# Kernel optimization log

Hardware: AMD Instinct MI355X
Metric: run time of the kernel (lower is better)

The kernel has to match this reference:

```python
import jax, jax.numpy as jnp
import numpy as np


def conv2d(x, w, pad=1):
    return jax.lax.conv_general_dilated(
        x, w, (1, 1), [(pad, pad), (pad, pad)],
        dimension_numbers=('NCHW', 'OIHW', 'NCHW'))


def bn(x, g, b, m, v, eps=1e-5):
    inv = g / jnp.sqrt(v + eps)
    return x * inv[None, :, None, None] + (b - m * inv)[None, :, None, None]


def deform_conv(x, wp, bp, wd):
    # v2-style DeformConv2D: internal p_conv -> offsets, bilinear sample, 3x3 conv
    b, c, h, w = x.shape
    ks = 3
    N = ks * ks
    offset = conv2d(x, wp, 1) + bp[None, :, None, None]   # (b, 2N, h, w)
    xp = jnp.pad(x, ((0, 0), (0, 0), (1, 1), (1, 1)))     # zero_padding(1)
    Hp, Wp = h + 2, w + 2
    off = offset.transpose(0, 2, 3, 1)                    # (b, h, w, 2N)
    pn_y, pn_x = jnp.meshgrid(jnp.arange(-1, 2), jnp.arange(-1, 2), indexing='ij')
    # sampling locations p = p_0 + p_n + offset (in padded coords)
    py = jnp.arange(1, h + 1)[None, :, None, None] + pn_y.reshape(-1)[None, None, None, :] + off[..., :N]
    px = jnp.arange(1, w + 1)[None, None, :, None] + pn_x.reshape(-1)[None, None, None, :] + off[..., N:]
    fy = jnp.floor(jax.lax.stop_gradient(py))
    fx = jnp.floor(jax.lax.stop_gradient(px))
    qy0 = jnp.clip(fy, 0, Hp - 1); qy1 = jnp.clip(fy + 1, 0, Hp - 1)
    qx0 = jnp.clip(fx, 0, Wp - 1); qx1 = jnp.clip(fx + 1, 0, Wp - 1)
    py = jnp.clip(py, 0, Hp - 1); px = jnp.clip(px, 0, Wp - 1)
    g_lt = (1 + (qy0 - py)) * (1 + (qx0 - px))
    g_rb = (1 - (qy1 - py)) * (1 - (qx1 - px))
    g_lb = (1 + (qy0 - py)) * (1 - (qx1 - px))
    g_rt = (1 - (qy1 - py)) * (1 + (qx0 - px))
    flat = xp.reshape(b, c, Hp * Wp)

    def gather(qy, qx):
        idx = (qy * Wp + qx).astype(jnp.int32).reshape(b, 1, -1)
        return jnp.take_along_axis(flat, idx, axis=2).reshape(b, c, h, w, N)

    x_off = (g_lt[:, None] * gather(qy0, qx0) + g_rb[:, None] * gather(qy1, qx1)
             + g_lb[:, None] * gather(qy0, qx1) + g_rt[:, None] * gather(qy1, qx0))
    outc = wd.shape[0]
    # equivalent to _reshape_x_offset + Conv2d(kernel=ks, stride=ks)
    return jnp.einsum('bchwn,ocn->bohw', x_off, wd.reshape(outc, c, N))


def setup_inputs() -> dict:
    key = jax.random.key(0)
    ks = jax.random.split(key, 24)
    B, H, W = 256, 28, 28

    def nrm(k, s, sc=1.0):
        return jax.random.normal(k, s, jnp.float32) * sc

    return {
        'x': nrm(ks[0], (B, 3, H, W)),
        'w1': nrm(ks[1], (32, 3, 3, 3), 0.2),
        'g1': jax.random.uniform(ks[2], (32,), jnp.float32) + 0.5,
        'b1': nrm(ks[3], (32,), 0.1),
        'm1': nrm(ks[4], (32,), 0.1),
        'v1': jax.random.uniform(ks[5], (32,), jnp.float32) + 0.5,
        'wp': nrm(ks[6], (18, 32, 3, 3), 0.01),  # p_conv: small offsets
        'bp': nrm(ks[7], (18,), 0.1),
        'w2': nrm(ks[8], (32, 32, 3, 3), 0.1),
        'g2': jax.random.uniform(ks[9], (32,), jnp.float32) + 0.5,
        'b2': nrm(ks[10], (32,), 0.1),
        'm2': nrm(ks[11], (32,), 0.1),
        'v2': jax.random.uniform(ks[12], (32,), jnp.float32) + 0.5,
        'w3': nrm(ks[13], (64, 32, 3, 3), 0.1),
        'g3': jax.random.uniform(ks[14], (64,), jnp.float32) + 0.5,
        'b3': nrm(ks[15], (64,), 0.1),
        'm3': nrm(ks[16], (64,), 0.1),
        'v3': jax.random.uniform(ks[17], (64,), jnp.float32) + 0.5,
        'wc': nrm(ks[18], (10, 64), 0.1),
        'bc': nrm(ks[19], (10,), 0.1),
    }


def reference(x, w1, g1, b1, m1, v1, wp, bp, w2, g2, b2, m2, v2,
              w3, g3, b3, m3, v3, wc, bc):
    h = bn(jax.nn.relu(conv2d(x, w1)), g1, b1, m1, v1)
    h = bn(jax.nn.relu(deform_conv(h, wp, bp, w2)), g2, b2, m2, v2)
    h = bn(jax.nn.relu(conv2d(h, w3)), g3, b3, m3, v3)
    h = h.mean(axis=(2, 3))               # avg_pool2d(28) on 28x28 -> global mean
    logits = h @ wc.T + bc
    return jax.nn.log_softmax(logits, axis=1)
```

## Files before the change

### kernel.cpp

```cpp
#include <hip/hip_runtime.h>
#include <hip/hip_bf16.h>
#include <math.h>

typedef __attribute__((ext_vector_type(8))) short short8;
typedef __attribute__((ext_vector_type(8))) _Float16 half8;
typedef __attribute__((ext_vector_type(4))) float floatx4;

#define NB 256
#define NW 12
#define NT (NW * 64)

#define WPB_OFF 0u
#define W2B_OFF 18432u
#define W3B_OFF 36864u
#define W1B_OFF 73728u
#define C1S_OFF 75776u
#define C2S_OFF 75904u
#define C3S_OFF 76032u

#define L_IMG1 0
#define L_U    50240
#define L_OFFT 100480
#define L_WL   125056
#define L_TOT  162944


#define LDS_FENCE() __asm__ volatile("" ::: "memory")

static __device__ __forceinline__ unsigned short f2h(float f) {
    _Float16 h = (_Float16)f;
    unsigned short u;
    __builtin_memcpy(&u, &h, 2);
    return u;
}
static __device__ __forceinline__ float h2f(unsigned short u) {
    _Float16 h;
    __builtin_memcpy(&h, &u, 2);
    return (float)h;
}

static __device__ __forceinline__ unsigned pkh(float a, float b) {
    _Float16 ha = (_Float16)a, hb = (_Float16)b;
    unsigned short ua, ub;
    __builtin_memcpy(&ua, &ha, 2);
    __builtin_memcpy(&ub, &hb, 2);
    return (unsigned)ua | ((unsigned)ub << 16);
}

static __device__ __forceinline__ half8 h8(uint4 u) {
    half8 r;
    __builtin_memcpy(&r, &u, 16);
    return r;
}

static __device__ __forceinline__ unsigned pkmul_l(unsigned a, unsigned b) {
    unsigned d;
    asm("v_pk_mul_f16 %0, %1, %2 op_sel:[0,0] op_sel_hi:[0,1]"
        : "=v"(d) : "v"(a), "v"(b));
    return d;
}
static __device__ __forceinline__ unsigned pkfma_l(unsigned a, unsigned b, unsigned c) {
    unsigned d;
    asm("v_pk_fma_f16 %0, %1, %2, %3 op_sel:[0,0,0] op_sel_hi:[0,1,1]"
        : "=v"(d) : "v"(a), "v"(b), "v"(c));
    return d;
}
static __device__ __forceinline__ unsigned pkfma_h(unsigned a, unsigned b, unsigned c) {
    unsigned d;
    asm("v_pk_fma_f16 %0, %1, %2, %3 op_sel:[1,0,0] op_sel_hi:[1,1,1]"
        : "=v"(d) : "v"(a), "v"(b), "v"(c));
    return d;
}

__global__ void wcvt(const float* __restrict__ wp, const float* __restrict__ w2,
                     const float* __restrict__ w3, const float* __restrict__ w1,
                     const float* __restrict__ g1, const float* __restrict__ b1,
                     const float* __restrict__ m1, const float* __restrict__ v1,
                     const float* __restrict__ g2, const float* __restrict__ b2,
                     const float* __restrict__ m2, const float* __restrict__ v2,
                     const float* __restrict__ g3, const float* __restrict__ b3,
                     const float* __restrict__ m3, const float* __restrict__ v3,
                     unsigned short* __restrict__ wpb, unsigned short* __restrict__ w2b,
                     unsigned short* __restrict__ w3b, unsigned short* __restrict__ w1b,
                     float* __restrict__ c1s, float* __restrict__ c2s,
                     float* __restrict__ c3s)
{
    int t = blockIdx.x * 256 + threadIdx.x;
    if (t < 9216) {
        int oc = t / 288, k = t % 288;
        int n = k >> 5, ic = k & 31;
        wpb[t] = (oc < 18) ? f2h(wp[oc * 288 + ic * 9 + n]) : (unsigned short)0;
    } else if (t < 18432) {
        int i = t - 9216;
        int oc = i / 288, k = i % 288;
        int n = k >> 5, ic = k & 31;
        float inv = g2[oc] * rsqrtf(v2[oc] + 1e-5f);
        w2b[i] = f2h(w2[oc * 288 + ic * 9 + n] * inv);
    } else if (t < 36864) {
        int i = t - 18432;
        int oc = i / 288, k = i % 288;
        int n = k >> 5, ic = k & 31;
        float inv = g3[oc] * rsqrtf(v3[oc] + 1e-5f);
        w3b[i] = f2h(w3[oc * 288 + ic * 9 + n] * inv);
    } else if (t < 37888) {
        int i = t - 36864;
        int oc = i >> 5, k = i & 31;
        int n = k / 3, ic = k - n * 3;
        float inv = g1[oc] * rsqrtf(v1[oc] + 1e-5f);
        w1b[i] = (k < 27) ? f2h(w1[oc * 27 + ic * 9 + n] * inv) : (unsigned short)0;
    } else if (t < 37920) {
        int c = t - 37888;
        float inv = g1[c] * rsqrtf(v1[c] + 1e-5f);
        c1s[c] = b1[c] - m1[c] * inv;
    } else if (t < 37952) {
        int c = t - 37920;
        float inv = g2[c] * rsqrtf(v2[c] + 1e-5f);
        c2s[c] = b2[c] - m2[c] * inv;
    } else if (t < 38016) {
        int c = t - 37952;
        float inv = g3[c] * rsqrtf(v3[c] + 1e-5f);
        c3s[c] = b3[c] - m3[c] * inv;
    }
}

__global__ __launch_bounds__(NT, 3) void meganet(
    const float* __restrict__ x,
    const unsigned short* __restrict__ wpb, const unsigned short* __restrict__ w2b,
    const unsigned short* __restrict__ w3b, const unsigned short* __restrict__ w1b,
    const float* __restrict__ c1s, const float* __restrict__ c2s,
    const float* __restrict__ c3s, const float* __restrict__ bp,
    const float* __restrict__ wc, const float* __restrict__ bc,
    float* __restrict__ outp)
{
    __shared__ __align__(16) unsigned char ALL[L_TOT];
    int t = threadIdx.x, b = blockIdx.x;
    int w = t >> 6, l = t & 63, col = l & 15, q = l >> 4;
    int qs = q << 4;
    int chxA = ((col >> 3) << 4) | ((col & 7) * 2);
    int chxB = ((((16 + col) >> 3) & 3) << 4) | ((col & 7) * 2);

    unsigned char* img1 = ALL + L_IMG1;
    unsigned char* uimg = ALL + L_U;

    {
        const float4* xg = (const float4*)(x + (size_t)b * 2352);
        float4* xl = (float4*)uimg;
        for (int i = t; i < 588; i += NT) xl[i] = xg[i];
    }
    {
        const uint4* s1 = (const uint4*)wpb;
        const uint4* s2 = (const uint4*)w2b;
        for (int i = t; i < 2304; i += NT) {
            int row = i / 36, g = i - row * 36;
            uint4 v = (row < 32) ? s1[row * 36 + g] : s2[(row - 32) * 36 + g];
            *(uint4*)(ALL + L_WL + row * 592 + g * 16) = v;
        }
        if (t < 128) *(uint4*)(ALL + L_OFFT + t * 16) = ((const uint4*)w1b)[t];
    }
    if (t == 700) ((float*)uimg)[2352] = 0.f;
    if (t < 4)  *(uint4*)(img1 + 784 * 64 + t * 16) = make_uint4(0u, 0u, 0u, 0u);
    if (t >= 4 && t < 8) *(uint4*)(uimg + 784 * 64 + (t - 4) * 16) = make_uint4(0u, 0u, 0u, 0u);

    float s0 = c1s[col], s1v = c1s[16 + col];
    float bias0 = bp[col];
    float bias1 = (col < 2) ? bp[16 + col] : 0.f;
    float sh0 = c2s[col], sh1 = c2s[16 + col];

    __syncthreads();

    {
        half8 bf0 = h8(*(const uint4*)(ALL + L_OFFT + col * 64 + q * 16));
        half8 bf1 = h8(*(const uint4*)(ALL + L_OFFT + (16 + col) * 64 + q * 16));
        const float* xs = (const float*)uimg;
        for (int mt = w; mt < 49; mt += NW) {
            int p = mt * 16 + col;
            int y = p / 28, xx = p % 28;
            unsigned au[4];
#pragma unroll
            for (int jp = 0; jp < 4; jp++) {
                float vv[2];
#pragma unroll
                for (int h = 0; h < 2; h++) {
                    int k = q * 8 + jp * 2 + h;
                    int n = k / 3, ic = k - n * 3;
                    int yy = y + n / 3 - 1, xc = xx + n % 3 - 1;
                    bool ok = (k < 27) && ((unsigned)yy < 28u) && ((unsigned)xc < 28u);
                    int idx = ok ? (ic * 784 + yy * 28 + xc) : 2352;
                    vv[h] = xs[idx];
                }
                au[jp] = pkh(vv[0], vv[1]);
            }
            uint4 a4 = make_uint4(au[0], au[1], au[2], au[3]);
            half8 a = h8(a4);
            floatx4 d0 = {0.f, 0.f, 0.f, 0.f}, d1 = {0.f, 0.f, 0.f, 0.f};
            d0 = __builtin_amdgcn_mfma_f32_16x16x32_f16(a, bf0, d0, 0, 0, 0);
            d1 = __builtin_amdgcn_mfma_f32_16x16x32_f16(a, bf1, d1, 0, 0, 0);
#pragma unroll
            for (int r = 0; r < 4; r++) {
                int pout = mt * 16 + q * 4 + r;
                int sp = (pout << 6) | ((pout & 6) << 3);
                *(unsigned short*)(img1 + (sp ^ chxA)) = f2h(fmaxf(d0[r], 0.f) + s0);
                *(unsigned short*)(img1 + (sp ^ chxB)) = f2h(fmaxf(d1[r], 0.f) + s1v);
            }
        }
    }
    __syncthreads();

    {
        const unsigned char* ib = img1;
        unsigned char* wsc = ALL + L_OFFT + w * 1536;
        unsigned short* otw = (unsigned short*)wsc;
        unsigned char* gscr = wsc + 576;

        half8 b2fr[18];
#pragma unroll
        for (int n = 0; n < 9; n++) {
            b2fr[n]     = h8(*(const uint4*)(ALL + L_WL + (32 + col) * 592 + n * 64 + q * 16));
            b2fr[9 + n] = h8(*(const uint4*)(ALL + L_WL + (48 + col) * 592 + n * 64 + q * 16));
        }

        for (int mt = w; mt < 49; mt += NW) {
            int p = mt * 16 + col;
            int y = p / 28, xx = p % 28;

            floatx4 a0 = {0.f, 0.f, 0.f, 0.f}, a1 = {0.f, 0.f, 0.f, 0.f};
#pragma unroll
            for (int n = 0; n < 9; n++) {
                int yy = y + n / 3 - 1, xc = xx + n % 3 - 1;
                bool ok = ((unsigned)yy < 28u) && ((unsigned)xc < 28u);
                int tp = ok ? (yy * 28 + xc) : 784;
                int sp = (tp << 6) | ((tp & 6) << 3);
                half8 a  = h8(*(const uint4*)(ib + (sp ^ qs)));
                half8 p0 = h8(*(const uint4*)(ALL + L_WL + col * 592 + n * 64 + q * 16));
                half8 p1 = h8(*(const uint4*)(ALL + L_WL + (16 + col) * 592 + n * 64 + q * 16));
                a0 = __builtin_amdgcn_mfma_f32_16x16x32_f16(a, p0, a0, 0, 0, 0);
                a1 = __builtin_amdgcn_mfma_f32_16x16x32_f16(a, p1, a1, 0, 0, 0);
            }
#pragma unroll
            for (int r = 0; r < 4; r++)
                otw[(q * 4 + r) * 18 + col] = f2h(a0[r] + bias0);
            if (col < 2) {
#pragma unroll
                for (int r = 0; r < 4; r++)
                    otw[(q * 4 + r) * 18 + 16 + col] = f2h(a1[r] + bias1);
            }
            LDS_FENCE();

            floatx4 d0 = {0.f, 0.f, 0.f, 0.f}, d1 = {0.f, 0.f, 0.f, 0.f};
#pragma unroll
            for (int tg = 0; tg < 3; tg++) {
                if (l < 48) {
                    int px = l & 15, n = tg * 3 + (l >> 4);
                    int pg = mt * 16 + px;
                    int yg = pg / 28, xg = pg % 28;
                    float offy = h2f(otw[px * 18 + n]);
                    float offx = h2f(otw[px * 18 + 9 + n]);
                    float py = (float)(yg + n / 3) + offy;
                    float pxf = (float)(xg + n % 3) + offx;
                    float fy = floorf(py), fx = floorf(pxf);
                    float qy0 = fminf(fmaxf(fy, 0.f), 29.f);
                    float qy1 = fminf(fmaxf(fy + 1.f, 0.f), 29.f);
                    float qx0 = fminf(fmaxf(fx, 0.f), 29.f);
                    float qx1 = fminf(fmaxf(fx + 1.f, 0.f), 29.f);
                    float pyc = fminf(fmaxf(py, 0.f), 29.f);
                    float pxc = fminf(fmaxf(pxf, 0.f), 29.f);
                    float glt = (1.f + (qy0 - pyc)) * (1.f + (qx0 - pxc));
                    float grb = (1.f - (qy1 - pyc)) * (1.f - (qx1 - pxc));
                    float glb = (1.f + (qy0 - pyc)) * (1.f - (qx1 - pxc));
                    float grt = (1.f - (qy1 - pyc)) * (1.f + (qx0 - pxc));
                    int iy0 = (int)qy0, iy1 = (int)qy1, ix0 = (int)qx0, ix1 = (int)qx1;
                    int ly0 = iy0 - 1, ly1 = iy1 - 1, lx0 = ix0 - 1, lx1 = ix1 - 1;
                    bool v00 = ((unsigned)ly0 < 28u) && ((unsigned)lx0 < 28u);
                    bool v11 = ((unsigned)ly1 < 28u) && ((unsigned)lx1 < 28u);
                    bool v01 = ((unsigned)ly0 < 28u) && ((unsigned)lx1 < 28u);
                    bool v10 = ((unsigned)ly1 < 28u) && ((unsigned)lx0 < 28u);
                    unsigned p00 = v00 ? (unsigned)(ly0 * 28 + lx0) : 784u;
                    unsigned p11 = v11 ? (unsigned)(ly1 * 28 + lx1) : 784u;
                    unsigned p01 = v01 ? (unsigned)(ly0 * 28 + lx1) : 784u;
                    unsigned p10 = v10 ? (unsigned)(ly1 * 28 + lx0) : 784u;
                    unsigned s00 = (p00 << 6) | ((p00 & 6u) << 3);
                    unsigned s11 = (p11 << 6) | ((p11 & 6u) << 3);
                    unsigned s01 = (p01 << 6) | ((p01 & 6u) << 3);
                    unsigned s10 = (p10 << 6) | ((p10 & 6u) << 3);
                    uint4 rec = make_uint4(pkh(glt, grb), pkh(glb, grt),
                                           s00 | (s11 << 16), s01 | (s10 << 16));
                    *(uint4*)(gscr + l * 16) = rec;
                }
                LDS_FENCE();

#pragma unroll
                for (int k3 = 0; k3 < 3; k3++) {
                    int n = tg * 3 + k3;
                    uint4 rec = *(const uint4*)(gscr + (k3 * 16 + col) * 16);
                    unsigned o00 = (rec.z & 0xffffu) ^ qs, o11 = (rec.z >> 16) ^ qs;
                    unsigned o01 = (rec.w & 0xffffu) ^ qs, o10 = (rec.w >> 16) ^ qs;
                    uint4 u00 = *(const uint4*)(ib + o00);
                    uint4 u11 = *(const uint4*)(ib + o11);
                    uint4 u01 = *(const uint4*)(ib + o01);
                    uint4 u10 = *(const uint4*)(ib + o10);
                    unsigned f0 = pkfma_h(rec.y, u10.x,
                                  pkfma_l(rec.y, u01.x,
                                  pkfma_h(rec.x, u11.x,
                                  pkmul_l(rec.x, u00.x))));
                    unsigned f1 = pkfma_h(rec.y, u10.y,
                                  pkfma_l(rec.y, u01.y,
                                  pkfma_h(rec.x, u11.y,
                                  pkmul_l(rec.x, u00.y))));
                    unsigned f2 = pkfma_h(rec.y, u10.z,
                                  pkfma_l(rec.y, u01.z,
                                  pkfma_h(rec.x, u11.z,
                                  pkmul_l(rec.x, u00.z))));
                    unsigned f3 = pkfma_h(rec.y, u10.w,
                                  pkfma_l(rec.y, u01.w,
                                  pkfma_h(rec.x, u11.w,
                                  pkmul_l(rec.x, u00.w))));
                    uint4 af4 = make_uint4(f0, f1, f2, f3);
                    half8 af = h8(af4);
                    d0 = __builtin_amdgcn_mfma_f32_16x16x32_f16(af, b2fr[n], d0, 0, 0, 0);
                    d1 = __builtin_amdgcn_mfma_f32_16x16x32_f16(af, b2fr[9 + n], d1, 0, 0, 0);
                }
            }
#pragma unroll
            for (int r = 0; r < 4; r++) {
                int pout = mt * 16 + q * 4 + r;
                int sp = (pout << 6) | ((pout & 6) << 3);
                *(unsigned short*)(uimg + (sp ^ chxA)) = f2h(fmaxf(d0[r], 0.f) + sh0);
                *(unsigned short*)(uimg + (sp ^ chxB)) = f2h(fmaxf(d1[r], 0.f) + sh1);
            }
        }
    }
    __syncthreads();

    {
        const uint4* src = (const uint4*)w3b;
        for (int i = t; i < 2304; i += NT) {
            int row = i / 36, g = i - row * 36;
            *(uint4*)(ALL + L_WL + row * 592 + g * 16) = src[row * 36 + g];
        }
    }
    __syncthreads();

    {
        float* part = (float*)(ALL + L_OFFT);
        int ocp = w & 1;
        const unsigned char* ib = uimg;

        half8 wfr[18];
#pragma unroll
        for (int n = 0; n < 9; n++) {
            wfr[n]     = h8(*(const uint4*)(ALL + L_WL + (ocp * 32 + col) * 592 + n * 64 + q * 16));
            wfr[9 + n] = h8(*(const uint4*)(ALL + L_WL + (ocp * 32 + 16 + col) * 592 + n * 64 + q * 16));
        }

        float psA = 0.f, psB = 0.f;
        for (int mt = (w >> 1); mt < 49; mt += (NW / 2)) {
            int p = mt * 16 + col;
            int y = p / 28, xx = p % 28;
            floatx4 cA = {0.f, 0.f, 0.f, 0.f}, cB = {0.f, 0.f, 0.f, 0.f};
#pragma unroll
            for (int n = 0; n < 9; n++) {
                int yy = y + n / 3 - 1, xc = xx + n % 3 - 1;
                bool ok = ((unsigned)yy < 28u) && ((unsigned)xc < 28u);
                int tp = ok ? (yy * 28 + xc) : 784;
                int sp = (tp << 6) | ((tp & 6) << 3);
                half8 a = h8(*(const uint4*)(ib + (sp ^ qs)));
                cA = __builtin_amdgcn_mfma_f32_16x16x32_f16(a, wfr[n], cA, 0, 0, 0);
                cB = __builtin_amdgcn_mfma_f32_16x16x32_f16(a, wfr[9 + n], cB, 0, 0, 0);
            }
            psA += fmaxf(cA[0], 0.f) + fmaxf(cA[1], 0.f) + fmaxf(cA[2], 0.f) + fmaxf(cA[3], 0.f);
            psB += fmaxf(cB[0], 0.f) + fmaxf(cB[1], 0.f) + fmaxf(cB[2], 0.f) + fmaxf(cB[3], 0.f);
        }
        psA += __shfl_xor(psA, 16, 64); psA += __shfl_xor(psA, 32, 64);
        psB += __shfl_xor(psB, 16, 64); psB += __shfl_xor(psB, 32, 64);
        if (l < 16) { part[w * 32 + l] = psA; part[w * 32 + 16 + l] = psB; }
    }
    __syncthreads();

    if (t < 64) {
        const float* part = (const float*)(ALL + L_OFFT);
        int hi = t >> 5, c = t & 31;
        float s = 0.f;
#pragma unroll
        for (int j = 0; j < NW / 2; j++) s += part[(2 * j + hi) * 32 + c];
        float feat = s * (1.f / 784.f) + c3s[t];
        float lg[10];
        float mx = -1e30f;
#pragma unroll
        for (int j = 0; j < 10; j++) {
            float v = feat * wc[j * 64 + t];
            v += __shfl_xor(v, 1, 64);  v += __shfl_xor(v, 2, 64);
            v += __shfl_xor(v, 4, 64);  v += __shfl_xor(v, 8, 64);
            v += __shfl_xor(v, 16, 64); v += __shfl_xor(v, 32, 64);
            lg[j] = v + bc[j];
            mx = fmaxf(mx, lg[j]);
        }
        float se = 0.f;
#pragma unroll
        for (int j = 0; j < 10; j++) se += expf(lg[j] - mx);
        float lse = logf(se);
#pragma unroll
        for (int j = 0; j < 10; j++)
            if (t == j) outp[(size_t)b * 10 + j] = lg[j] - mx - lse;
    }
}

extern "C" void kernel_launch(void* const* d_in, const int* in_sizes, int n_in,
                              void* d_out, int out_size, void* d_ws, size_t ws_size,
                              hipStream_t stream)
{
    (void)in_sizes; (void)n_in; (void)out_size; (void)ws_size;
    const float* x  = (const float*)d_in[0];
    const float* w1 = (const float*)d_in[1];
    const float* g1 = (const float*)d_in[2];
    const float* b1 = (const float*)d_in[3];
    const float* m1 = (const float*)d_in[4];
    const float* v1 = (const float*)d_in[5];
    const float* wp = (const float*)d_in[6];
    const float* bp = (const float*)d_in[7];
    const float* w2 = (const float*)d_in[8];
    const float* g2 = (const float*)d_in[9];
    const float* b2 = (const float*)d_in[10];
    const float* m2 = (const float*)d_in[11];
    const float* v2 = (const float*)d_in[12];
    const float* w3 = (const float*)d_in[13];
    const float* g3 = (const float*)d_in[14];
    const float* b3 = (const float*)d_in[15];
    const float* m3 = (const float*)d_in[16];
    const float* v3 = (const float*)d_in[17];
    const float* wc = (const float*)d_in[18];
    const float* bc = (const float*)d_in[19];
    float* outp = (float*)d_out;

    unsigned char* ws = (unsigned char*)d_ws;
    unsigned short* wpb = (unsigned short*)(ws + WPB_OFF);
    unsigned short* w2b = (unsigned short*)(ws + W2B_OFF);
    unsigned short* w3b = (unsigned short*)(ws + W3B_OFF);
    unsigned short* w1b = (unsigned short*)(ws + W1B_OFF);
    float* c1s = (float*)(ws + C1S_OFF);
    float* c2s = (float*)(ws + C2S_OFF);
    float* c3s = (float*)(ws + C3S_OFF);

    wcvt<<<149, 256, 0, stream>>>(wp, w2, w3, w1, g1, b1, m1, v1,
                                  g2, b2, m2, v2, g3, b3, m3, v3,
                                  wpb, w2b, w3b, w1b, c1s, c2s, c3s);
    meganet<<<NB, NT, 0, stream>>>(x, wpb, w2b, w3b, w1b, c1s, c2s, c3s,
                                   bp, wc, bc, outp);
}
```

Before: 128.1 us.

## Share conv3 A-fragment across all 64 outputs and transpose offset scratch layout

The conv3 stage now has each wave compute all four 16-channel output groups for a tile, reading weights from LDS per tap instead of splitting output channels across wave pairs. This reuses the activation fragment four times and halves redundant A loads. In the offset conv, p0 weights are hoisted into registers, p1 loads are limited to the two useful lanes, and offsets are stored channel-major with vector stores. The cost is more LDS weight traffic per MFMA in conv3 and a different work split across waves (49 tiles over 12 waves).

New measurement: 134.5 us. 1.05x slower.

```diff
diff --git a/kernel.cpp b/kernel.cpp
--- a/kernel.cpp
+++ b/kernel.cpp
@@ -5,6 +5,7 @@
 typedef __attribute__((ext_vector_type(8))) short short8;
 typedef __attribute__((ext_vector_type(8))) _Float16 half8;
 typedef __attribute__((ext_vector_type(4))) float floatx4;
+typedef __attribute__((ext_vector_type(4))) unsigned short ushort4v;
 
 #define NB 256
 #define NW 12
@@ -23,6 +24,7 @@
 #define L_OFFT 100480
 #define L_WL   125056
 #define L_TOT  162944
+
 
 
 #define LDS_FENCE() __asm__ volatile("" ::: "memory")
@@ -213,8 +215,10 @@
         unsigned char* gscr = wsc + 576;
 
         half8 b2fr[18];
+        half8 p0fr[9];
 #pragma unroll
         for (int n = 0; n < 9; n++) {
+            p0fr[n]     = h8(*(const uint4*)(ALL + L_WL + col * 592 + n * 64 + q * 16));
             b2fr[n]     = h8(*(const uint4*)(ALL + L_WL + (32 + col) * 592 + n * 64 + q * 16));
             b2fr[9 + n] = h8(*(const uint4*)(ALL + L_WL + (48 + col) * 592 + n * 64 + q * 16));
         }
@@ -230,19 +234,24 @@
                 bool ok = ((unsigned)yy < 28u) && ((unsigned)xc < 28u);
                 int tp = ok ? (yy * 28 + xc) : 784;
                 int sp = (tp << 6) | ((tp & 6) << 3);
-                half8 a  = h8(*(const uint4*)(ib + (sp ^ qs)));
-                half8 p0 = h8(*(const uint4*)(ALL + L_WL + col * 592 + n * 64 + q * 16));
-                half8 p1 = h8(*(const uint4*)(ALL + L_WL + (16 + col) * 592 + n * 64 + q * 16));
-                a0 = __builtin_amdgcn_mfma_f32_16x16x32_f16(a, p0, a0, 0, 0, 0);
-                a1 = __builtin_amdgcn_mfma_f32_16x16x32_f16(a, p1, a1, 0, 0, 0);
-            }
-#pragma unroll
-            for (int r = 0; r < 4; r++)
-                otw[(q * 4 + r) * 18 + col] = f2h(a0[r] + bias0);
-            if (col < 2) {
-#pragma unroll
-                for (int r = 0; r < 4; r++)
-                    otw[(q * 4 + r) * 18 + 16 + col] = f2h(a1[r] + bias1);
+                half8 a = h8(*(const uint4*)(ib + (sp ^ qs)));
+                a0 = __builtin_amdgcn_mfma_f32_16x16x32_f16(a, p0fr[n], a0, 0, 0, 0);
+                half8 p1v = h8(make_uint4(0u, 0u, 0u, 0u));
+                if (col < 2)
+                    p1v = h8(*(const uint4*)(ALL + L_WL + (16 + col) * 592 + n * 64 + q * 16));
+                a1 = __builtin_amdgcn_mfma_f32_16x16x32_f16(a, p1v, a1, 0, 0, 0);
+            }
+            {
+                ushort4v ov;
+                ov[0] = f2h(a0[0] + bias0); ov[1] = f2h(a0[1] + bias0);
+                ov[2] = f2h(a0[2] + bias0); ov[3] = f2h(a0[3] + bias0);
+                *(ushort4v*)(otw + col * 16 + q * 4) = ov;
+                if (col < 2) {
+                    ushort4v ov1;
+                    ov1[0] = f2h(a1[0] + bias1); ov1[1] = f2h(a1[1] + bias1);
+                    ov1[2] = f2h(a1[2] + bias1); ov1[3] = f2h(a1[3] + bias1);
+                    *(ushort4v*)(otw + (16 + col) * 16 + q * 4) = ov1;
+                }
             }
             LDS_FENCE();
 
@@ -253,8 +262,8 @@
                     int px = l & 15, n = tg * 3 + (l >> 4);
                     int pg = mt * 16 + px;
                     int yg = pg / 28, xg = pg % 28;
-                    float offy = h2f(otw[px * 18 + n]);
-                    float offx = h2f(otw[px * 18 + 9 + n]);
+                    float offy = h2f(otw[n * 16 + px]);
+                    float offx = h2f(otw[(9 + n) * 16 + px]);
                     float py = (float)(yg + n / 3) + offy;
                     float pxf = (float)(xg + n % 3) + offx;
                     float fy = floorf(py), fx = floorf(pxf);
@@ -342,21 +351,14 @@
 
     {
         float* part = (float*)(ALL + L_OFFT);
-        int ocp = w & 1;
         const unsigned char* ib = uimg;
 
-        half8 wfr[18];
-#pragma unroll
-        for (int n = 0; n < 9; n++) {
-            wfr[n]     = h8(*(const uint4*)(ALL + L_WL + (ocp * 32 + col) * 592 + n * 64 + q * 16));
-            wfr[9 + n] = h8(*(const uint4*)(ALL + L_WL + (ocp * 32 + 16 + col) * 592 + n * 64 + q * 16));
-        }
-
-        float psA = 0.f, psB = 0.f;
-        for (int mt = (w >> 1); mt < 49; mt += (NW / 2)) {
+        float ps0 = 0.f, ps1 = 0.f, ps2 = 0.f, ps3 = 0.f;
+        for (int mt = w; mt < 49; mt += NW) {
             int p = mt * 16 + col;
             int y = p / 28, xx = p % 28;
-            floatx4 cA = {0.f, 0.f, 0.f, 0.f}, cB = {0.f, 0.f, 0.f, 0.f};
+            floatx4 c0 = {0.f, 0.f, 0.f, 0.f}, c1 = {0.f, 0.f, 0.f, 0.f};
+            floatx4 c2 = {0.f, 0.f, 0.f, 0.f}, c3 = {0.f, 0.f, 0.f, 0.f};
 #pragma unroll
             for (int n = 0; n < 9; n++) {
                 int yy = y + n / 3 - 1, xc = xx + n % 3 - 1;
@@ -364,24 +366,38 @@
                 int tp = ok ? (yy * 28 + xc) : 784;
                 int sp = (tp << 6) | ((tp & 6) << 3);
                 half8 a = h8(*(const uint4*)(ib + (sp ^ qs)));
-                cA = __builtin_amdgcn_mfma_f32_16x16x32_f16(a, wfr[n], cA, 0, 0, 0);
-                cB = __builtin_amdgcn_mfma_f32_16x16x32_f16(a, wfr[9 + n], cB, 0, 0, 0);
-            }
-            psA += fmaxf(cA[0], 0.f) + fmaxf(cA[1], 0.f) + fmaxf(cA[2], 0.f) + fmaxf(cA[3], 0.f);
-            psB += fmaxf(cB[0], 0.f) + fmaxf(cB[1], 0.f) + fmaxf(cB[2], 0.f) + fmaxf(cB[3], 0.f);
-        }
-        psA += __shfl_xor(psA, 16, 64); psA += __shfl_xor(psA, 32, 64);
-        psB += __shfl_xor(psB, 16, 64); psB += __shfl_xor(psB, 32, 64);
-        if (l < 16) { part[w * 32 + l] = psA; part[w * 32 + 16 + l] = psB; }
+                half8 w0 = h8(*(const uint4*)(ALL + L_WL + col * 592 + n * 64 + q * 16));
+                half8 w1 = h8(*(const uint4*)(ALL + L_WL + (16 + col) * 592 + n * 64 + q * 16));
+                half8 w2v = h8(*(const uint4*)(ALL + L_WL + (32 + col) * 592 + n * 64 + q * 16));
+                half8 w3v = h8(*(const uint4*)(ALL + L_WL + (48 + col) * 592 + n * 64 + q * 16));
+                c0 = __builtin_amdgcn_mfma_f32_16x16x32_f16(a, w0, c0, 0, 0, 0);
+                c1 = __builtin_amdgcn_mfma_f32_16x16x32_f16(a, w1, c1, 0, 0, 0);
+                c2 = __builtin_amdgcn_mfma_f32_16x16x32_f16(a, w2v, c2, 0, 0, 0);
+                c3 = __builtin_amdgcn_mfma_f32_16x16x32_f16(a, w3v, c3, 0, 0, 0);
+            }
+            ps0 += fmaxf(c0[0], 0.f) + fmaxf(c0[1], 0.f) + fmaxf(c0[2], 0.f) + fmaxf(c0[3], 0.f);
+            ps1 += fmaxf(c1[0], 0.f) + fmaxf(c1[1], 0.f) + fmaxf(c1[2], 0.f) + fmaxf(c1[3], 0.f);
+            ps2 += fmaxf(c2[0], 0.f) + fmaxf(c2[1], 0.f) + fmaxf(c2[2], 0.f) + fmaxf(c2[3], 0.f);
+            ps3 += fmaxf(c3[0], 0.f) + fmaxf(c3[1], 0.f) + fmaxf(c3[2], 0.f) + fmaxf(c3[3], 0.f);
+        }
+        ps0 += __shfl_xor(ps0, 16, 64); ps0 += __shfl_xor(ps0, 32, 64);
+        ps1 += __shfl_xor(ps1, 16, 64); ps1 += __shfl_xor(ps1, 32, 64);
+        ps2 += __shfl_xor(ps2, 16, 64); ps2 += __shfl_xor(ps2, 32, 64);
+        ps3 += __shfl_xor(ps3, 16, 64); ps3 += __shfl_xor(ps3, 32, 64);
+        if (l < 16) {
+            part[w * 64 + l]      = ps0;
+            part[w * 64 + 16 + l] = ps1;
+            part[w * 64 + 32 + l] = ps2;
+            part[w * 64 + 48 + l] = ps3;
+        }
     }
     __syncthreads();
 
     if (t < 64) {
         const float* part = (const float*)(ALL + L_OFFT);
-        int hi = t >> 5, c = t & 31;
         float s = 0.f;
 #pragma unroll
-        for (int j = 0; j < NW / 2; j++) s += part[(2 * j + hi) * 32 + c];
+        for (int j = 0; j < NW; j++) s += part[j * 64 + t];
         float feat = s * (1.f / 784.f) + c3s[t];
         float lg[10];
         float mx = -1e30f;
```
